# Kernel tuning notes

Measured on AMD Instinct MI355X. Metric: run time of the kernel, lower is better.

Reference implementation:

```python
import jax, jax.numpy as jnp
import numpy as np

D_MODEL = 512
NUM_HEADS = 8
HEAD_DIM = D_MODEL // NUM_HEADS
ATTN_WINDOW = 256


def setup_inputs() -> dict:
    key = jax.random.key(0)
    ks = jax.random.split(key, 5)
    B, S = 2, 4096
    x = jax.random.normal(ks[0], (B, S, D_MODEL), dtype=jnp.float32)
    s = 1.0 / np.sqrt(D_MODEL)
    qkv_w = jax.random.uniform(ks[1], (3 * D_MODEL, D_MODEL), minval=-s, maxval=s, dtype=jnp.float32)
    qkv_b = jax.random.uniform(ks[2], (3 * D_MODEL,), minval=-s, maxval=s, dtype=jnp.float32)
    out_w = jax.random.uniform(ks[3], (D_MODEL, D_MODEL), minval=-s, maxval=s, dtype=jnp.float32)
    out_b = jax.random.uniform(ks[4], (D_MODEL,), minval=-s, maxval=s, dtype=jnp.float32)
    return {"x": x, "qkv_w": qkv_w, "qkv_b": qkv_b, "out_w": out_w, "out_b": out_b}


def reference(x, qkv_w, qkv_b, out_w, out_b):
    B, S, D = x.shape
    scale = HEAD_DIM ** (-0.5)
    qkv = x @ qkv_w.T + qkv_b                       # [B,S,3D]
    qkv = qkv.reshape(B, S, 3, NUM_HEADS, HEAD_DIM)
    q, k, v = qkv[:, :, 0], qkv[:, :, 1], qkv[:, :, 2]
    scores = jnp.einsum('bthd,bshd->bhts', q, k) * scale  # [B,H,S,S]
    i = jnp.arange(S)[:, None]
    j = jnp.arange(S)[None, :]
    # causal AND within sliding window of size ATTN_WINDOW
    mask = (j <= i) & (j >= i - ATTN_WINDOW)        # [S,S] bool
    scores = jnp.where(mask, scores, -jnp.inf)
    weights = jax.nn.softmax(scores, axis=-1)
    out = jnp.einsum('bhts,bshd->bthd', weights, v).reshape(B, S, D)
    return out @ out_w.T + out_b
```

## Files before the change

### kernel.cpp

```cpp
#include <hip/hip_runtime.h>

#define S_LEN 4096
#define BATCH 2
#define DM 512
#define NH 8
#define DH 64
#define WINDOW 256

typedef __bf16 bf16x8 __attribute__((ext_vector_type(8)));
typedef float f32x4 __attribute__((ext_vector_type(4)));
typedef unsigned short u16x8 __attribute__((ext_vector_type(8)));

typedef const __attribute__((address_space(1))) unsigned int* gas_ptr;
typedef __attribute__((address_space(3))) unsigned int* las_ptr;

#define SCALE_LOG2E 0.1803368801111204f

__device__ __forceinline__ unsigned short f2bf(float f) {
  unsigned int u = __float_as_uint(f);
  u += 0x7fffu + ((u >> 16) & 1u);
  return (unsigned short)(u >> 16);
}

#define N4_X (8192 * 512 / 4)
#define N4_QW (1536 * 512 / 4)
#define N4_OW (512 * 512 / 4)
__global__ __launch_bounds__(256) void convert_all(const float* __restrict__ x,
                                                   const float* __restrict__ qw,
                                                   const float* __restrict__ ow,
                                                   unsigned short* __restrict__ dst) {
  const int i = blockIdx.x * blockDim.x + threadIdx.x;
  const float4* src;
  int off;
  if (i < N4_X) { src = (const float4*)x; off = 0; }
  else if (i < N4_X + N4_QW) { src = (const float4*)qw; off = N4_X; }
  else { src = (const float4*)ow; off = N4_X + N4_QW; }
  const float4 v = src[i - off];
  ushort4 o;
  o.x = f2bf(v.x); o.y = f2bf(v.y); o.z = f2bf(v.z); o.w = f2bf(v.w);
  ((ushort4*)dst)[i] = o;
}

__device__ __forceinline__ void gemm_core(const unsigned short* __restrict__ A,
                                          const unsigned short* __restrict__ Bm,
                                          int m0, int n0,
                                          unsigned short* sA, unsigned short* sB,
                                          f32x4 acc[4][4]) {
  const int t = threadIdx.x;
  const int wave = t >> 6, lane = t & 63;
  const int wr = wave >> 1, wc = wave & 1;
  const int quad = lane >> 4, l16 = lane & 15;

  for (int k0 = 0; k0 < 512; k0 += 32) {
#pragma unroll
    for (int p = 0; p < 2; ++p) {
      const int ci = wave * 128 + p * 64 + lane;
      const int row = ci >> 2, cg = ci & 3;
      const unsigned short* ga = A + (size_t)(m0 + row) * 512 + k0 + cg * 8;
      __builtin_amdgcn_global_load_lds((gas_ptr)(const void*)ga,
                                       (las_ptr)(void*)(sA + wave * 1024 + p * 512), 16, 0, 0);
      const unsigned short* gb = Bm + (size_t)(n0 + row) * 512 + k0 + cg * 8;
      __builtin_amdgcn_global_load_lds((gas_ptr)(const void*)gb,
                                       (las_ptr)(void*)(sB + wave * 1024 + p * 512), 16, 0, 0);
    }
    __syncthreads();
    bf16x8 af[4], bff[4];
#pragma unroll
    for (int i = 0; i < 4; ++i)
      af[i] = *(const bf16x8*)&sA[(wr * 64 + i * 16 + l16) * 32 + quad * 8];
#pragma unroll
    for (int j = 0; j < 4; ++j)
      bff[j] = *(const bf16x8*)&sB[(wc * 64 + j * 16 + l16) * 32 + quad * 8];
#pragma unroll
    for (int i = 0; i < 4; ++i)
#pragma unroll
      for (int j = 0; j < 4; ++j)
        acc[i][j] = __builtin_amdgcn_mfma_f32_16x16x32_bf16(af[i], bff[j], acc[i][j], 0, 0, 0);
    __syncthreads();
  }
}

__global__ __launch_bounds__(256) void gemm_qkv(const unsigned short* __restrict__ xb,
                                                const unsigned short* __restrict__ wb,
                                                const float* __restrict__ bias,
                                                unsigned short* __restrict__ Qb,
                                                unsigned short* __restrict__ Kb,
                                                unsigned short* __restrict__ Vt) {
  __shared__ __align__(16) unsigned short sA[128 * 32];
  __shared__ __align__(16) unsigned short sB[128 * 32];
  f32x4 acc[4][4] = {};
  const int m0 = blockIdx.y * 128, n0 = blockIdx.x * 128;
  gemm_core(xb, wb, m0, n0, sA, sB, acc);

  const int t = threadIdx.x;
  const int wave = t >> 6, lane = t & 63;
  const int wr = wave >> 1, wc = wave & 1;
  const int quad = lane >> 4, l16 = lane & 15;
#pragma unroll
  for (int j = 0; j < 4; ++j) {
    const int n = n0 + wc * 64 + j * 16 + l16;
    const float bv = bias[n];
#pragma unroll
    for (int i = 0; i < 4; ++i) {
      const int mr = m0 + wr * 64 + i * 16 + quad * 4;
      if (n < DM) {
#pragma unroll
        for (int r = 0; r < 4; ++r)
          Qb[(size_t)(mr + r) * DM + n] = f2bf(acc[i][j][r] + bv);
      } else if (n < 2 * DM) {
#pragma unroll
        for (int r = 0; r < 4; ++r)
          Kb[(size_t)(mr + r) * DM + (n - DM)] = f2bf(acc[i][j][r] + bv);
      } else {
        const int d = n & 63, h = (n - 2 * DM) >> 6;
#pragma unroll
        for (int r = 0; r < 4; ++r) {
          const int m = mr + r;
          const int b = m >> 12, s = m & (S_LEN - 1);
          Vt[((size_t)((b * NH + h) * DH + d)) * S_LEN + s] = f2bf(acc[i][j][r] + bv);
        }
      }
    }
  }
}

__global__ __launch_bounds__(256) void gemm_out(const unsigned short* __restrict__ Ab,
                                                const unsigned short* __restrict__ wb,
                                                const float* __restrict__ bias,
                                                float* __restrict__ C) {
  __shared__ __align__(16) unsigned short sA[128 * 32];
  __shared__ __align__(16) unsigned short sB[128 * 32];
  f32x4 acc[4][4] = {};
  const int m0 = blockIdx.y * 128, n0 = blockIdx.x * 128;
  gemm_core(Ab, wb, m0, n0, sA, sB, acc);

  const int t = threadIdx.x;
  const int wave = t >> 6, lane = t & 63;
  const int wr = wave >> 1, wc = wave & 1;
  const int quad = lane >> 4, l16 = lane & 15;
#pragma unroll
  for (int j = 0; j < 4; ++j) {
    const int n = n0 + wc * 64 + j * 16 + l16;
    const float bv = bias[n];
#pragma unroll
    for (int i = 0; i < 4; ++i) {
      const int mr = m0 + wr * 64 + i * 16 + quad * 4;
#pragma unroll
      for (int r = 0; r < 4; ++r)
        C[(size_t)(mr + r) * DM + n] = acc[i][j][r] + bv;
    }
  }
}

__global__ __launch_bounds__(256) void attn_mfma(const unsigned short* __restrict__ Qb,
                                                 const unsigned short* __restrict__ Kb,
                                                 const unsigned short* __restrict__ Vt,
                                                 unsigned short* __restrict__ AO) {
  __shared__ __align__(16) unsigned short Qs[64 * 72];
  __shared__ __align__(16) unsigned short Ks[64 * 72];
  __shared__ __align__(16) unsigned short Vs[64 * 72];
  __shared__ __align__(16) unsigned short Ps[64 * 72];
  const int t = threadIdx.x;
  const int wave = t >> 6, lane = t & 63;
  const int quad = lane >> 4, l16 = lane & 15;
  const int q0 = blockIdx.x * 64, h = blockIdx.y, b = blockIdx.z;

  const unsigned short* Kbase = Kb + (size_t)b * S_LEN * DM + h * DH;
  const unsigned short* Vbase = Vt + (size_t)((b * NH + h) * DH) * S_LEN;

#pragma unroll
  for (int s = 0; s < 2; ++s) {
    const int f = t + 256 * s;
    const int row = f >> 3, cg = f & 7;
    *(u16x8*)&Qs[row * 72 + cg * 8] =
        *(const u16x8*)(Qb + (size_t)(b * S_LEN + q0 + row) * DM + h * DH + cg * 8);
  }

  const int first = (q0 >= WINDOW) ? 0 : (4 - blockIdx.x);

  u16x8 kbuf[2][2], vbuf[2][2];
#define LOAD_CHUNK(c0, p)                                                      \
  do {                                                                         \
    _Pragma("unroll") for (int s = 0; s < 2; ++s) {                            \
      const int f = t + 256 * s;                                               \
      const int row = f >> 3, c8 = f & 7;                                      \
      kbuf[p][s] = *(const u16x8*)(Kbase + (size_t)((c0) + row) * DM + c8 * 8);\
      vbuf[p][s] = *(const u16x8*)(Vbase + (size_t)row * S_LEN + (c0) + c8 * 8);\
    }                                                                          \
  } while (0)

#pragma unroll
  for (int c = 0; c < 5; ++c)
    if (c == first) LOAD_CHUNK(q0 - WINDOW + c * 64, c & 1);

  float m_[4], l_[4];
  f32x4 O[4] = {};
#pragma unroll
  for (int r = 0; r < 4; ++r) { m_[r] = -1e30f; l_[r] = 0.f; }

#pragma unroll
  for (int c = 0; c < 5; ++c) {
    if (c < first) continue;
    const int c0 = q0 - WINDOW + c * 64;
    __syncthreads();
#pragma unroll
    for (int s = 0; s < 2; ++s) {
      const int f = t + 256 * s;
      const int row = f >> 3, c8 = f & 7;
      *(u16x8*)&Ks[row * 72 + c8 * 8] = kbuf[c & 1][s];
      *(u16x8*)&Vs[row * 72 + c8 * 8] = vbuf[c & 1][s];
    }
    if (c < 4) LOAD_CHUNK(c0 + 64, (c + 1) & 1);
    __syncthreads();

    bf16x8 aq0 = *(const bf16x8*)&Qs[(wave * 16 + l16) * 72 + quad * 8];
    bf16x8 aq1 = *(const bf16x8*)&Qs[(wave * 16 + l16) * 72 + 32 + quad * 8];
    f32x4 sc[4];
#pragma unroll
    for (int nt = 0; nt < 4; ++nt) {
      bf16x8 bk0 = *(const bf16x8*)&Ks[(nt * 16 + l16) * 72 + quad * 8];
      bf16x8 bk1 = *(const bf16x8*)&Ks[(nt * 16 + l16) * 72 + 32 + quad * 8];
      f32x4 z = {};
      z = __builtin_amdgcn_mfma_f32_16x16x32_bf16(aq0, bk0, z, 0, 0, 0);
      sc[nt] = __builtin_amdgcn_mfma_f32_16x16x32_bf16(aq1, bk1, z, 0, 0, 0);
    }

    float rmax[4];
#pragma unroll
    for (int r = 0; r < 4; ++r) rmax[r] = -1e30f;
#pragma unroll
    for (int nt = 0; nt < 4; ++nt) {
      const int jj = nt * 16 + l16;
#pragma unroll
      for (int r = 0; r < 4; ++r) {
        const int ii = wave * 16 + quad * 4 + r;
        float v = sc[nt][r] * SCALE_LOG2E;
        if (c == 0) v = (jj >= ii) ? v : -1e30f;
        if (c == 4) v = (jj <= ii) ? v : -1e30f;
        sc[nt][r] = v;
        rmax[r] = fmaxf(rmax[r], v);
      }
    }
#pragma unroll
    for (int off = 1; off <= 8; off <<= 1)
#pragma unroll
      for (int r = 0; r < 4; ++r) rmax[r] = fmaxf(rmax[r], __shfl_xor(rmax[r], off));

    float alpha[4], csum[4];
#pragma unroll
    for (int r = 0; r < 4; ++r) {
      const float mn = fmaxf(m_[r], rmax[r]);
      alpha[r] = exp2f(m_[r] - mn);
      m_[r] = mn;
      float su = 0.f;
#pragma unroll
      for (int nt = 0; nt < 4; ++nt) {
        const float p = exp2f(sc[nt][r] - mn);
        sc[nt][r] = p;
        su += p;
      }
      csum[r] = su;
    }
#pragma unroll
    for (int off = 1; off <= 8; off <<= 1)
#pragma unroll
      for (int r = 0; r < 4; ++r) csum[r] += __shfl_xor(csum[r], off);
#pragma unroll
    for (int r = 0; r < 4; ++r) l_[r] = l_[r] * alpha[r] + csum[r];

#pragma unroll
    for (int nt = 0; nt < 4; ++nt)
#pragma unroll
      for (int r = 0; r < 4; ++r)
        Ps[(wave * 16 + quad * 4 + r) * 72 + nt * 16 + l16] = f2bf(sc[nt][r]);

    bf16x8 ap0 = *(const bf16x8*)&Ps[(wave * 16 + l16) * 72 + quad * 8];
    bf16x8 ap1 = *(const bf16x8*)&Ps[(wave * 16 + l16) * 72 + 32 + quad * 8];
#pragma unroll
    for (int nt = 0; nt < 4; ++nt) {
#pragma unroll
      for (int r = 0; r < 4; ++r) O[nt][r] *= alpha[r];
      bf16x8 bv0 = *(const bf16x8*)&Vs[(nt * 16 + l16) * 72 + quad * 8];
      bf16x8 bv1 = *(const bf16x8*)&Vs[(nt * 16 + l16) * 72 + 32 + quad * 8];
      O[nt] = __builtin_amdgcn_mfma_f32_16x16x32_bf16(ap0, bv0, O[nt], 0, 0, 0);
      O[nt] = __builtin_amdgcn_mfma_f32_16x16x32_bf16(ap1, bv1, O[nt], 0, 0, 0);
    }
  }

#pragma unroll
  for (int r = 0; r < 4; ++r) l_[r] = 1.f / l_[r];
#pragma unroll
  for (int nt = 0; nt < 4; ++nt) {
    const int col = h * DH + nt * 16 + l16;
#pragma unroll
    for (int r = 0; r < 4; ++r) {
      const int m = b * S_LEN + q0 + wave * 16 + quad * 4 + r;
      AO[(size_t)m * DM + col] = f2bf(O[nt][r] * l_[r]);
    }
  }
}

extern "C" void kernel_launch(void* const* d_in, const int* in_sizes, int n_in,
                              void* d_out, int out_size, void* d_ws, size_t ws_size,
                              hipStream_t stream) {
  const float* x = (const float*)d_in[0];
  const float* qkv_w = (const float*)d_in[1];
  const float* qkv_b = (const float*)d_in[2];
  const float* out_w = (const float*)d_in[3];
  const float* out_b = (const float*)d_in[4];
  float* out = (float*)d_out;

  const int M = BATCH * S_LEN;
  unsigned short* ws = (unsigned short*)d_ws;
  unsigned short* xb   = ws;
  unsigned short* wqkv = xb + (size_t)M * DM;
  unsigned short* wout = wqkv + 3 * DM * DM;
  unsigned short* Qb   = wout + DM * DM;
  unsigned short* Kb   = Qb + (size_t)M * DM;
  unsigned short* Vt   = Kb + (size_t)M * DM;
  unsigned short* AO   = Vt + (size_t)M * DM;

  convert_all<<<(N4_X + N4_QW + N4_OW) / 256, 256, 0, stream>>>(x, qkv_w, out_w, xb);

  gemm_qkv<<<dim3(3 * DM / 128, M / 128), 256, 0, stream>>>(xb, wqkv, qkv_b, Qb, Kb, Vt);

  attn_mfma<<<dim3(S_LEN / 64, NH, BATCH), 256, 0, stream>>>(Qb, Kb, Vt, AO);

  gemm_out<<<dim3(DM / 128, M / 128), 256, 0, stream>>>(AO, wout, out_b, out);
}
```

Before: 149.7 us.

## Deepen GEMM K-step, swizzle block order, stage V transpose via LDS

The GEMM core now loads a 64-wide K slice per barrier pair instead of 32, which halves the number of synchronizations. The QKV and output GEMMs remap a 1D grid into grouped 8-row tiles for better L2 reuse. The V-transposed epilogue is staged through shared memory so the global writes become coalesced 16-byte stores. The attention grid is also remapped so that blocks with different heads and query tiles interleave across XCDs. Together these add index arithmetic and more shared memory per block, which may lower occupancy.

```diff
diff --git a/kernel.cpp b/kernel.cpp
--- a/kernel.cpp
+++ b/kernel.cpp
@@ -51,33 +51,45 @@
   const int wr = wave >> 1, wc = wave & 1;
   const int quad = lane >> 4, l16 = lane & 15;
 
-  for (int k0 = 0; k0 < 512; k0 += 32) {
-#pragma unroll
-    for (int p = 0; p < 2; ++p) {
-      const int ci = wave * 128 + p * 64 + lane;
-      const int row = ci >> 2, cg = ci & 3;
-      const unsigned short* ga = A + (size_t)(m0 + row) * 512 + k0 + cg * 8;
+  for (int k0 = 0; k0 < 512; k0 += 64) {
+#pragma unroll
+    for (int p = 0; p < 4; ++p) {
+      const int g = wave * 4 + p;
+      const int kk = g >> 3;
+      const int row = (g & 7) * 16 + (lane >> 2);
+      const int col = (lane & 3) * 8;
+      const unsigned short* ga = A + (size_t)(m0 + row) * 512 + k0 + kk * 32 + col;
       __builtin_amdgcn_global_load_lds((gas_ptr)(const void*)ga,
-                                       (las_ptr)(void*)(sA + wave * 1024 + p * 512), 16, 0, 0);
-      const unsigned short* gb = Bm + (size_t)(n0 + row) * 512 + k0 + cg * 8;
+                                       (las_ptr)(void*)(sA + g * 512), 16, 0, 0);
+      const unsigned short* gb = Bm + (size_t)(n0 + row) * 512 + k0 + kk * 32 + col;
       __builtin_amdgcn_global_load_lds((gas_ptr)(const void*)gb,
-                                       (las_ptr)(void*)(sB + wave * 1024 + p * 512), 16, 0, 0);
+                                       (las_ptr)(void*)(sB + g * 512), 16, 0, 0);
     }
     __syncthreads();
-    bf16x8 af[4], bff[4];
-#pragma unroll
-    for (int i = 0; i < 4; ++i)
-      af[i] = *(const bf16x8*)&sA[(wr * 64 + i * 16 + l16) * 32 + quad * 8];
-#pragma unroll
-    for (int j = 0; j < 4; ++j)
-      bff[j] = *(const bf16x8*)&sB[(wc * 64 + j * 16 + l16) * 32 + quad * 8];
-#pragma unroll
-    for (int i = 0; i < 4; ++i)
+#pragma unroll
+    for (int kk = 0; kk < 2; ++kk) {
+      bf16x8 af[4], bff[4];
+#pragma unroll
+      for (int i = 0; i < 4; ++i)
+        af[i] = *(const bf16x8*)&sA[kk * 4096 + (wr * 64 + i * 16 + l16) * 32 + quad * 8];
 #pragma unroll
       for (int j = 0; j < 4; ++j)
-        acc[i][j] = __builtin_amdgcn_mfma_f32_16x16x32_bf16(af[i], bff[j], acc[i][j], 0, 0, 0);
+        bff[j] = *(const bf16x8*)&sB[kk * 4096 + (wc * 64 + j * 16 + l16) * 32 + quad * 8];
+#pragma unroll
+      for (int i = 0; i < 4; ++i)
+#pragma unroll
+        for (int j = 0; j < 4; ++j)
+          acc[i][j] = __builtin_amdgcn_mfma_f32_16x16x32_bf16(af[i], bff[j], acc[i][j], 0, 0, 0);
+    }
     __syncthreads();
   }
+}
+
+__device__ __forceinline__ void swz(int id, int nbn, int& r, int& c) {
+  const int x = id & 7;
+  const int t2 = id >> 3;
+  c = t2 % nbn;
+  r = (t2 / nbn) * 8 + x;
 }
 
 __global__ __launch_bounds__(256) void gemm_qkv(const unsigned short* __restrict__ xb,
@@ -86,39 +98,64 @@
                                                 unsigned short* __restrict__ Qb,
                                                 unsigned short* __restrict__ Kb,
                                                 unsigned short* __restrict__ Vt) {
-  __shared__ __align__(16) unsigned short sA[128 * 32];
-  __shared__ __align__(16) unsigned short sB[128 * 32];
+  __shared__ __align__(16) unsigned short smem[16384];
   f32x4 acc[4][4] = {};
-  const int m0 = blockIdx.y * 128, n0 = blockIdx.x * 128;
-  gemm_core(xb, wb, m0, n0, sA, sB, acc);
+  int rb, cb;
+  swz(blockIdx.x, 12, rb, cb);
+  const int m0 = rb * 128, n0 = cb * 128;
+  gemm_core(xb, wb, m0, n0, smem, smem + 8192, acc);
 
   const int t = threadIdx.x;
   const int wave = t >> 6, lane = t & 63;
   const int wr = wave >> 1, wc = wave & 1;
   const int quad = lane >> 4, l16 = lane & 15;
-#pragma unroll
-  for (int j = 0; j < 4; ++j) {
-    const int n = n0 + wc * 64 + j * 16 + l16;
-    const float bv = bias[n];
-#pragma unroll
-    for (int i = 0; i < 4; ++i) {
-      const int mr = m0 + wr * 64 + i * 16 + quad * 4;
-      if (n < DM) {
-#pragma unroll
-        for (int r = 0; r < 4; ++r)
-          Qb[(size_t)(mr + r) * DM + n] = f2bf(acc[i][j][r] + bv);
-      } else if (n < 2 * DM) {
-#pragma unroll
-        for (int r = 0; r < 4; ++r)
-          Kb[(size_t)(mr + r) * DM + (n - DM)] = f2bf(acc[i][j][r] + bv);
-      } else {
-        const int d = n & 63, h = (n - 2 * DM) >> 6;
-#pragma unroll
-        for (int r = 0; r < 4; ++r) {
-          const int m = mr + r;
-          const int b = m >> 12, s = m & (S_LEN - 1);
-          Vt[((size_t)((b * NH + h) * DH + d)) * S_LEN + s] = f2bf(acc[i][j][r] + bv);
+
+  if (n0 < 2 * DM) {
+#pragma unroll
+    for (int j = 0; j < 4; ++j) {
+      const int n = n0 + wc * 64 + j * 16 + l16;
+      const float bv = bias[n];
+#pragma unroll
+      for (int i = 0; i < 4; ++i) {
+        const int mr = m0 + wr * 64 + i * 16 + quad * 4;
+        if (n < DM) {
+#pragma unroll
+          for (int r = 0; r < 4; ++r)
+            Qb[(size_t)(mr + r) * DM + n] = f2bf(acc[i][j][r] + bv);
+        } else {
+#pragma unroll
+          for (int r = 0; r < 4; ++r)
+            Kb[(size_t)(mr + r) * DM + (n - DM)] = f2bf(acc[i][j][r] + bv);
         }
+      }
+    }
+  } else {
+    const int bb = m0 >> 12, s0 = m0 & (S_LEN - 1);
+    const int h0 = (n0 - 2 * DM) >> 6;
+    unsigned short* T = smem;
+#pragma unroll
+    for (int hh = 0; hh < 2; ++hh) {
+      __syncthreads();
+      if (wc == hh) {
+#pragma unroll
+        for (int j = 0; j < 4; ++j) {
+          const int d = j * 16 + l16;
+          const float bv = bias[n0 + hh * 64 + j * 16 + l16];
+#pragma unroll
+          for (int i = 0; i < 4; ++i)
+#pragma unroll
+            for (int r = 0; r < 4; ++r)
+              T[d * 136 + wr * 64 + i * 16 + quad * 4 + r] = f2bf(acc[i][j][r] + bv);
+        }
+      }
+      __syncthreads();
+      const int h = h0 + hh;
+#pragma unroll
+      for (int it = 0; it < 4; ++it) {
+        const int f = t + 256 * it;
+        const int d = f >> 4, c8 = f & 15;
+        *(u16x8*)(Vt + ((size_t)((bb * NH + h) * DH + d)) * S_LEN + s0 + c8 * 8) =
+            *(const u16x8*)&T[d * 136 + c8 * 8];
       }
     }
   }
@@ -128,11 +165,12 @@
                                                 const unsigned short* __restrict__ wb,
                                                 const float* __restrict__ bias,
                                                 float* __restrict__ C) {
-  __shared__ __align__(16) unsigned short sA[128 * 32];
-  __shared__ __align__(16) unsigned short sB[128 * 32];
+  __shared__ __align__(16) unsigned short smem[16384];
   f32x4 acc[4][4] = {};
-  const int m0 = blockIdx.y * 128, n0 = blockIdx.x * 128;
-  gemm_core(Ab, wb, m0, n0, sA, sB, acc);
+  int rb, cb;
+  swz(blockIdx.x, 4, rb, cb);
+  const int m0 = rb * 128, n0 = cb * 128;
+  gemm_core(Ab, wb, m0, n0, smem, smem + 8192, acc);
 
   const int t = threadIdx.x;
   const int wave = t >> 6, lane = t & 63;
@@ -163,7 +201,15 @@
   const int t = threadIdx.x;
   const int wave = t >> 6, lane = t & 63;
   const int quad = lane >> 4, l16 = lane & 15;
-  const int q0 = blockIdx.x * 64, h = blockIdx.y, b = blockIdx.z;
+
+  const int id = blockIdx.x;
+  const int X = id & 7;
+  int t2 = id >> 3;
+  const int o = t2 & 7; t2 >>= 3;
+  const int h = t2 & 7;
+  const int b = t2 >> 3;
+  const int qt = ((X - h) & 7) * 8 + o;
+  const int q0 = qt * 64;
 
   const unsigned short* Kbase = Kb + (size_t)b * S_LEN * DM + h * DH;
   const unsigned short* Vbase = Vt + (size_t)((b * NH + h) * DH) * S_LEN;
@@ -176,7 +222,7 @@
         *(const u16x8*)(Qb + (size_t)(b * S_LEN + q0 + row) * DM + h * DH + cg * 8);
   }
 
-  const int first = (q0 >= WINDOW) ? 0 : (4 - blockIdx.x);
+  const int first = (qt >= 4) ? 0 : (4 - qt);
 
   u16x8 kbuf[2][2], vbuf[2][2];
 #define LOAD_CHUNK(c0, p)                                                      \
@@ -322,9 +368,9 @@
 
   convert_all<<<(N4_X + N4_QW + N4_OW) / 256, 256, 0, stream>>>(x, qkv_w, out_w, xb);
 
-  gemm_qkv<<<dim3(3 * DM / 128, M / 128), 256, 0, stream>>>(xb, wqkv, qkv_b, Qb, Kb, Vt);
-
-  attn_mfma<<<dim3(S_LEN / 64, NH, BATCH), 256, 0, stream>>>(Qb, Kb, Vt, AO);
-
-  gemm_out<<<dim3(DM / 128, M / 128), 256, 0, stream>>>(AO, wout, out_b, out);
-}
+  gemm_qkv<<<768, 256, 0, stream>>>(xb, wqkv, qkv_b, Qb, Kb, Vt);
+
+  attn_mfma<<<1024, 256, 0, stream>>>(Qb, Kb, Vt, AO);
+
+  gemm_out<<<256, 256, 0, stream>>>(AO, wout, out_b, out);
+}
```

Measured after the change: 154.2 us. +3.0%, slower.
